# Performance work log

Measured on AMD Instinct MI355X. Metric: run time of the kernel, lower is better.

Reference implementation:

```python
import jax, jax.numpy as jnp
import numpy as np

D_MODEL = 1024
N_HEADS = 16
HEAD_DIM = D_MODEL // N_HEADS
D_FF = 4096
MAX_STEPS = 16
MAX_LEN = 64  # hardcoded in the module
LN_EPS = 1e-5


def _layer_norm(x, g, b):
    m = jnp.mean(x, axis=-1, keepdims=True)
    v = jnp.mean((x - m) ** 2, axis=-1, keepdims=True)
    return (x - m) * jax.lax.rsqrt(v + LN_EPS) * g + b


def setup_inputs() -> dict:
    key = jax.random.key(0)
    ks = jax.random.split(key, 12)
    B, S = 8, 1024
    std = 0.02
    return {
        "x": jax.random.normal(ks[0], (B, S, D_MODEL), dtype=jnp.float32),
        "step_embed": jax.random.normal(ks[1], (MAX_STEPS, D_MODEL), dtype=jnp.float32) * std,
        "qkv_w": jax.random.normal(ks[2], (D_MODEL, 3 * D_MODEL), dtype=jnp.float32) * std,
        "qkv_b": jnp.zeros((3 * D_MODEL,), dtype=jnp.float32),
        "out_w": jax.random.normal(ks[3], (D_MODEL, D_MODEL), dtype=jnp.float32) * std,
        "out_b": jnp.zeros((D_MODEL,), dtype=jnp.float32),
        "rel_pos_bias": jax.random.normal(ks[4], (2 * MAX_LEN - 1,), dtype=jnp.float32) * std,
        "w1": jax.random.normal(ks[5], (D_MODEL, D_FF), dtype=jnp.float32) * std,
        "b1": jnp.zeros((D_FF,), dtype=jnp.float32),
        "w2": jax.random.normal(ks[6], (D_FF, D_MODEL), dtype=jnp.float32) * std,
        "b2": jnp.zeros((D_MODEL,), dtype=jnp.float32),
        "ln1_g": jnp.ones((D_MODEL,), dtype=jnp.float32),
        "ln1_b": jnp.zeros((D_MODEL,), dtype=jnp.float32),
        "ln2_g": jnp.ones((D_MODEL,), dtype=jnp.float32),
        "ln2_b": jnp.zeros((D_MODEL,), dtype=jnp.float32),
        "think_step": 3,
    }


def reference(x, step_embed, qkv_w, qkv_b, out_w, out_b, rel_pos_bias,
              w1, b1, w2, b2, ln1_g, ln1_b, ln2_g, ln2_b, think_step):
    B, S, D = x.shape
    scale = HEAD_DIM ** -0.5

    # step embedding (clamped), broadcast over batch and sequence
    step = min(int(think_step), MAX_STEPS - 1)
    x = x + step_embed[step][None, None, :]

    # QKV projection -> (3, B, H, S, Dh)
    qkv = (x @ qkv_w + qkv_b).reshape(B, S, 3, N_HEADS, HEAD_DIM)
    qkv = jnp.transpose(qkv, (2, 0, 3, 1, 4))
    q, k, v = qkv[0], qkv[1], qkv[2]

    # attention scores with clamped relative-position bias
    scores = jnp.einsum("bhqd,bhkd->bhqk", q, k) * scale
    pos = jnp.arange(S)
    rel = jnp.clip(pos[:, None] - pos[None, :] + (MAX_LEN - 1), 0, 2 * MAX_LEN - 2)
    scores = scores + rel_pos_bias[rel][None, None, :, :]

    probs = jax.nn.softmax(scores, axis=-1)
    attn = jnp.einsum("bhqk,bhkd->bhqd", probs, v)
    attn = jnp.transpose(attn, (0, 2, 1, 3)).reshape(B, S, D)
    attn = attn @ out_w + out_b

    x = _layer_norm(x + attn, ln1_g, ln1_b)
    ffn = jax.nn.gelu(x @ w1 + b1, approximate=False) @ w2 + b2
    x = _layer_norm(x + ffn, ln2_g, ln2_b)
    return x
```

## Files before the change

kernel.cpp:

```cpp
#include <hip/hip_runtime.h>
#include <cstdint>
#include <cmath>

typedef unsigned short u16;
typedef unsigned int u32;
typedef __bf16 bf16x8 __attribute__((ext_vector_type(8)));
typedef float f32x4 __attribute__((ext_vector_type(4)));
typedef float f32x16 __attribute__((ext_vector_type(16)));

#define DEV __device__ __forceinline__

DEV u16 f2bf(float f) {
    union { float f; unsigned u; } a; a.f = f;
    unsigned u = a.u;
    return (u16)((u + 0x7FFFu + ((u >> 16) & 1u)) >> 16);
}

DEV u32 pack2bf(float a, float b) {
    union { float f; u32 u; } ua, ub; ua.f = a; ub.f = b;
    return __builtin_amdgcn_perm(ub.u + 0x8000u, ua.u + 0x8000u, 0x07060302u);
}

DEV float fast_exp2(float x) {
    float r;
    asm("v_exp_f32 %0, %1" : "=v"(r) : "v"(x));
    return r;
}

DEV float fast_rcp(float x) {
    float r;
    asm("v_rcp_f32 %0, %1" : "=v"(r) : "v"(x));
    return r;
}

DEV float gelu_fast(float v) {
    float z = fabsf(v) * 0.70710678118f;
    float t = fast_rcp(1.f + 0.3275911f * z);
    float poly = ((((1.061405429f * t - 1.453152027f) * t + 1.421413741f) * t
                   - 0.284496736f) * t + 0.254829592f) * t;
    float e = fast_exp2(-z * z * 1.44269504088896f);
    float erfv = 1.f - poly * e;
    erfv = copysignf(erfv, v);
    return 0.5f * v * (1.f + erfv);
}

DEV void async16(void* lds, const void* g) {
    __builtin_amdgcn_global_load_lds(
        (const __attribute__((address_space(1))) unsigned int*)g,
        (__attribute__((address_space(3))) unsigned int*)lds, 16, 0, 0);
}

#define LOG2E 1.44269504088896f
#define PHI()   __builtin_amdgcn_s_setprio(1)
#define PLO()   __builtin_amdgcn_s_setprio(0)

__global__ __launch_bounds__(256)
void prep_k(const float* __restrict__ s0, u16* __restrict__ d0,
            const float* __restrict__ s1, u16* __restrict__ d1,
            const float* __restrict__ s2, u16* __restrict__ d2,
            const float* __restrict__ s3, u16* __restrict__ d3,
            const float* __restrict__ x, const float* __restrict__ se,
            const int* __restrict__ ts, u16* __restrict__ xb) {
    int b = blockIdx.x, tid = threadIdx.x;
    if (b < 12288) {
        __shared__ float tile[32][33];
        const float* src; u16* dst; int N, tidx;
        if (b < 3072)      { src = s0; dst = d0; N = 3072; tidx = b; }
        else if (b < 4096) { src = s1; dst = d1; N = 1024; tidx = b - 3072; }
        else if (b < 8192) { src = s2; dst = d2; N = 4096; tidx = b - 4096; }
        else               { src = s3; dst = d3; N = 1024; tidx = b - 8192; }
        int ntx = N >> 5;
        int n0 = (tidx % ntx) * 32, k0 = (tidx / ntx) * 32;
        int K = (b >= 8192) ? 4096 : 1024;
        int tx = tid & 31, ty = tid >> 5;
        #pragma unroll
        for (int i = ty; i < 32; i += 8) tile[i][tx] = src[(size_t)(k0 + i) * N + n0 + tx];
        __syncthreads();
        #pragma unroll
        for (int i = ty; i < 32; i += 8) dst[(size_t)(n0 + i) * K + k0 + tx] = f2bf(tile[tx][i]);
    } else {
        int st = ts[0]; st = st < 0 ? 0 : (st > 15 ? 15 : st);
        size_t i = (size_t)(b - 12288) * 256 + tid;
        float4 v = ((const float4*)x)[i];
        int c = (int)(i & 255);
        float4 e = ((const float4*)(se + (size_t)st * 1024))[c];
        v.x += e.x; v.y += e.y; v.z += e.z; v.w += e.w;
        ushort4 u; u.x = f2bf(v.x); u.y = f2bf(v.y); u.z = f2bf(v.z); u.w = f2bf(v.w);
        ((ushort4*)xb)[i] = u;
    }
}

template<int EPI>
__global__ __launch_bounds__(256, 3)
void gemm_bt(const u16* __restrict__ A, const u16* __restrict__ Bt,
             const float* __restrict__ bias, int Kdim,
             u16* __restrict__ ob0, u16* __restrict__ ob1, u16* __restrict__ ob2,
             const float* __restrict__ addf, float* __restrict__ outf,
             const float* __restrict__ se_, const int* __restrict__ ts_) {
    __shared__ __align__(16) u16 lA[128 * 64];
    __shared__ __align__(16) u16 lB[128 * 64];
    const int tid = threadIdx.x, wave = tid >> 6, lane = tid & 63;
    const int m5 = lane & 31, h = lane >> 5;
    const int wm = wave >> 1, wn = wave & 1;
    const size_t m0 = (size_t)blockIdx.x * 128, n0 = (size_t)blockIdx.y * 128;
    const size_t kb = (size_t)Kdim * 2;

    f32x16 acc[2][2];
    #pragma unroll
    for (int i = 0; i < 2; i++)
        #pragma unroll
        for (int j = 0; j < 2; j++)
            #pragma unroll
            for (int e = 0; e < 16; e++) acc[i][j][e] = 0.f;

    const char* Ab = (const char*)A + m0 * kb;
    const char* Bb = (const char*)Bt + n0 * kb;

    auto stage = [&](const char* srcbase, u16* ldsb, int k0) {
        #pragma unroll
        for (int j = 0; j < 4; j++) {
            int loff = wave * 4096 + j * 1024 + lane * 16;
            int L = loff >> 4, r = L >> 3, c = L & 7, g = c ^ (r & 7);
            async16((char*)ldsb + loff, srcbase + (size_t)r * kb + (size_t)k0 * 2 + g * 16);
        }
    };

    stage(Ab, lA, 0); stage(Bb, lB, 0);
    const int r7 = m5 & 7;
    for (int k0 = 0; k0 < Kdim; k0 += 64) {
        __syncthreads();
        bf16x8 af[2][4], bfr[2][4];
        #pragma unroll
        for (int ti = 0; ti < 2; ti++) {
            int rowA = wm * 64 + ti * 32 + m5;
            int rowB = wn * 64 + ti * 32 + m5;
            #pragma unroll
            for (int kh = 0; kh < 4; kh++) {
                int cs = (kh * 2 + h) ^ r7;
                af[ti][kh]  = *(const bf16x8*)((const char*)lA + rowA * 128 + cs * 16);
                bfr[ti][kh] = *(const bf16x8*)((const char*)lB + rowB * 128 + cs * 16);
            }
        }
        __syncthreads();
        if (k0 + 64 < Kdim) { stage(Ab, lA, k0 + 64); stage(Bb, lB, k0 + 64); }
        #pragma unroll
        for (int kh = 0; kh < 4; kh++)
            #pragma unroll
            for (int ti = 0; ti < 2; ti++)
                #pragma unroll
                for (int tj = 0; tj < 2; tj++)
                    acc[ti][tj] = __builtin_amdgcn_mfma_f32_32x32x16_bf16(
                        af[ti][kh], bfr[tj][kh], acc[ti][tj], 0, 0, 0);
    }

    const float* serow = nullptr;
    if constexpr (EPI == 1) {
        int st = ts_[0]; st = st < 0 ? 0 : (st > 15 ? 15 : st);
        serow = se_ + (size_t)st * 1024;
    }

    #pragma unroll
    for (int ti = 0; ti < 2; ti++) {
        #pragma unroll
        for (int tj = 0; tj < 2; tj++) {
            size_t col = n0 + wn * 64 + tj * 32 + m5;
            float bv = bias[col];
            if constexpr (EPI == 0) {
                size_t t = col >> 10, c = col & 1023, hh = c >> 6, dh = c & 63;
                #pragma unroll
                for (int g = 0; g < 4; g++) {
                    size_t row0 = m0 + wm * 64 + ti * 32 + 4 * h + 8 * g;
                    size_t bq = row0 >> 10, s0 = row0 & 1023;
                    if (t == 0) {
                        #pragma unroll
                        for (int r = 0; r < 4; r++)
                            ob0[((bq * 16 + hh) * 1024 + s0 + r) * 64 + dh] =
                                f2bf((acc[ti][tj][g * 4 + r] + bv) * 0.18033688011112f);
                    } else if (t == 1) {
                        #pragma unroll
                        for (int r = 0; r < 4; r++)
                            ob1[((bq * 16 + hh) * 1024 + s0 + r) * 64 + dh] =
                                f2bf(acc[ti][tj][g * 4 + r] + bv);
                    } else {
                        ushort4 tmp;
                        tmp.x = f2bf(acc[ti][tj][g * 4 + 0] + bv);
                        tmp.y = f2bf(acc[ti][tj][g * 4 + 1] + bv);
                        tmp.z = f2bf(acc[ti][tj][g * 4 + 2] + bv);
                        tmp.w = f2bf(acc[ti][tj][g * 4 + 3] + bv);
                        *(ushort4*)(ob2 + ((bq * 16 + hh) * 64 + dh) * 1024 + s0) = tmp;
                    }
                }
            } else if constexpr (EPI == 1) {
                float sev = serow[col];
                #pragma unroll
                for (int g = 0; g < 4; g++)
                    #pragma unroll
                    for (int r = 0; r < 4; r++) {
                        size_t row = m0 + wm * 64 + ti * 32 + 4 * h + 8 * g + r;
                        float val = acc[ti][tj][g * 4 + r] + bv;
                        size_t o = row * 1024 + col;
                        outf[o] = addf[o] + sev + val;
                    }
            } else {
                #pragma unroll
                for (int g = 0; g < 4; g++) {
                    #pragma unroll
                    for (int r = 0; r < 4; r++) {
                        size_t row = m0 + wm * 64 + ti * 32 + 4 * h + 8 * g + r;
                        float val = acc[ti][tj][g * 4 + r] + bv;
                        if constexpr (EPI == 2) {
                            ob0[row * 4096 + col] = f2bf(gelu_fast(val));
                        } else {
                            size_t o = row * 1024 + col;
                            outf[o] = addf[o] + val;
                        }
                    }
                }
            }
        }
    }
}

__global__ __launch_bounds__(256, 2)
void attn_k(const u16* __restrict__ Q, const u16* __restrict__ K_, const u16* __restrict__ Vt,
            const float* __restrict__ relb, u16* __restrict__ Out) {
    __shared__ __align__(16) u16 sP[128 * 128];
    __shared__ __align__(16) u16 sK[128 * 64];
    __shared__ __align__(16) u16 sVt[64 * 128];
    __shared__ float sL[4][128];
    __shared__ float sLinv[128];
    __shared__ float sRel[128];

    const int tid = threadIdx.x, wave = tid >> 6, lane = tid & 63;
    const int m5 = lane & 31, h = lane >> 5;
    const int bh = blockIdx.x, q0 = blockIdx.y * 128;
    const size_t base = (size_t)bh * 65536;

    if (tid < 127) sRel[tid] = relb[tid] * LOG2E;

    auto stageK = [&](int kv0) {
        const char* kbp = (const char*)(K_ + base + (size_t)kv0 * 64);
        #pragma unroll
        for (int j = 0; j < 4; j++) {
            int loff = wave * 4096 + j * 1024 + lane * 16;
            int L = loff >> 4, r = L >> 3, c = L & 7, g = c ^ (r & 7);
            async16((char*)sK + loff, kbp + (size_t)r * 128 + g * 16);
        }
    };
    auto stageV = [&](int kv0) {
        const char* vbp = (const char*)(Vt + base) + (size_t)kv0 * 2;
        #pragma unroll
        for (int j = 0; j < 4; j++) {
            int loff = wave * 4096 + j * 1024 + lane * 16;
            int L = loff >> 4, r = L >> 4, c = L & 15, g = c ^ (r & 15);
            async16((char*)sVt + loff, vbp + (size_t)r * 2048 + g * 16);
        }
    };

    {
        const char* qb = (const char*)(Q + base + (size_t)q0 * 64);
        #pragma unroll
        for (int j = 0; j < 4; j++) {
            int loff = wave * 4096 + j * 1024 + lane * 16;
            int L = loff >> 4, r = L >> 3, c = L & 7, g = c ^ (r & 7);
            async16((char*)sP + loff, qb + (size_t)r * 128 + g * 16);
        }
    }
    stageK(0); stageV(0);
    __syncthreads();

    bf16x8 qf[4][4];
    #pragma unroll
    for (int qt = 0; qt < 4; qt++) {
        int row = qt * 32 + m5;
        #pragma unroll
        for (int s = 0; s < 4; s++) {
            int cs = (2 * s + h) ^ (m5 & 7);
            qf[qt][s] = *(const bf16x8*)((const char*)sP + row * 128 + cs * 16);
        }
    }
    __syncthreads();

    const int qh = wave >> 1, dhh = wave & 1;
    f32x16 Oacc[2];
    #pragma unroll
    for (int i = 0; i < 2; i++)
        #pragma unroll
        for (int e = 0; e < 16; e++) Oacc[i][e] = 0.f;
    float lsum[4] = {0.f, 0.f, 0.f, 0.f};

    for (int t = 0; t < 8; t++) {
        const int kv0 = t * 128;
        const int kvr = wave * 32 + m5;
        bf16x8 kf[4];
        #pragma unroll
        for (int s = 0; s < 4; s++) {
            int cs = (2 * s + h) ^ (m5 & 7);
            kf[s] = *(const bf16x8*)((const char*)sK + kvr * 128 + cs * 16);
        }
        f32x16 sc[4];
        #pragma unroll
        for (int qt = 0; qt < 4; qt++)
            #pragma unroll
            for (int e = 0; e < 16; e++) sc[qt][e] = 0.f;
        PHI();
        #pragma unroll
        for (int s = 0; s < 4; s++)
            #pragma unroll
            for (int qt = 0; qt < 4; qt++)
                sc[qt] = __builtin_amdgcn_mfma_f32_32x32x16_bf16(kf[s], qf[qt][s], sc[qt], 0, 0, 0);
        PLO();

        const int kvb = kv0 + wave * 32 + 4 * h;
        const bool far_lo = (kv0 >= q0 + 190);
        const bool far_hi = (kv0 <= q0 - 190);
        #pragma unroll
        for (int qt = 0; qt < 4; qt++) {
            const int qs = q0 + qt * 32 + m5;
            if (far_lo || far_hi) {
                float cb = far_lo ? sRel[0] : sRel[126];
                #pragma unroll
                for (int e = 0; e < 16; e++) sc[qt][e] = fast_exp2(sc[qt][e] + cb);
            } else {
                int relbase = qs - kvb + 63;
                #pragma unroll
                for (int g = 0; g < 4; g++)
                    #pragma unroll
                    for (int r = 0; r < 4; r++) {
                        int rel = relbase - 8 * g - r;
                        rel = rel < 0 ? 0 : (rel > 126 ? 126 : rel);
                        sc[qt][4 * g + r] = fast_exp2(sc[qt][4 * g + r] + sRel[rel]);
                    }
            }
            #pragma unroll
            for (int e = 0; e < 16; e++) lsum[qt] += sc[qt][e];
            u32 pk[4][2];
            #pragma unroll
            for (int g = 0; g < 4; g++) {
                pk[g][0] = pack2bf(sc[qt][4 * g + 0], sc[qt][4 * g + 1]);
                pk[g][1] = pack2bf(sc[qt][4 * g + 2], sc[qt][4 * g + 3]);
            }
            const int q = qt * 32 + m5;
            char* prow = (char*)sP + q * 256;
            #pragma unroll
            for (int u = 0; u < 2; u++) {
                u32 s0 = h ? pk[2 * u][0] : pk[2 * u + 1][0];
                u32 s1 = h ? pk[2 * u][1] : pk[2 * u + 1][1];
                u32 r0 = __shfl_xor((int)s0, 32);
                u32 r1 = __shfl_xor((int)s1, 32);
                uint4 w;
                if (h == 0) { w.x = pk[2 * u][0]; w.y = pk[2 * u][1]; w.z = r0; w.w = r1; }
                else        { w.x = r0; w.y = r1; w.z = pk[2 * u + 1][0]; w.w = pk[2 * u + 1][1]; }
                int c16 = (4 * wave + 2 * u + h) ^ (q & 15);
                *(uint4*)(prow + c16 * 16) = w;
            }
        }
        __syncthreads();
        if (t < 7) stageK(kv0 + 128);

        #pragma unroll
        for (int s = 0; s < 8; s++) {
            int dh = dhh * 32 + m5;
            int cv = (2 * s + h) ^ (dh & 15);
            bf16x8 vf = *(const bf16x8*)((const char*)sVt + dh * 256 + cv * 16);
            #pragma unroll
            for (int qt = 0; qt < 2; qt++) {
                int q = qh * 64 + qt * 32 + m5;
                int cp = (2 * s + h) ^ (q & 15);
                bf16x8 pf = *(const bf16x8*)((const char*)sP + q * 256 + cp * 16);
                PHI();
                Oacc[qt] = __builtin_amdgcn_mfma_f32_32x32x16_bf16(pf, vf, Oacc[qt], 0, 0, 0);
                PLO();
            }
        }
        __syncthreads();
        if (t < 7) stageV(kv0 + 128);
    }

    #pragma unroll
    for (int qt = 0; qt < 4; qt++) lsum[qt] += __shfl_xor(lsum[qt], 32);
    if (h == 0) {
        #pragma unroll
        for (int qt = 0; qt < 4; qt++) sL[wave][qt * 32 + m5] = lsum[qt];
    }
    __syncthreads();
    if (tid < 128) sLinv[tid] = 1.f / (sL[0][tid] + sL[1][tid] + sL[2][tid] + sL[3][tid]);
    __syncthreads();

    const int b = bh >> 4, hh = bh & 15;
    const int dh = dhh * 32 + m5;
    #pragma unroll
    for (int qt = 0; qt < 2; qt++) {
        #pragma unroll
        for (int g = 0; g < 4; g++) {
            #pragma unroll
            for (int r = 0; r < 4; r++) {
                int rl = qh * 64 + qt * 32 + 4 * h + 8 * g + r;
                float val = Oacc[qt][4 * g + r] * sLinv[rl];
                size_t s = (size_t)(q0 + rl);
                Out[((size_t)b * 1024 + s) * 1024 + hh * 64 + dh] = f2bf(val);
            }
        }
    }
}

template<bool WB>
__global__ __launch_bounds__(256)
void ln_k(const float* __restrict__ in, const float* __restrict__ g, const float* __restrict__ b,
          float* __restrict__ of, u16* __restrict__ ob) {
    __shared__ float ws1[4], ws2[4];
    int row = blockIdx.x, t = threadIdx.x;
    float4 v = ((const float4*)(in + (size_t)row * 1024))[t];
    float s = v.x + v.y + v.z + v.w;
    float s2 = v.x * v.x + v.y * v.y + v.z * v.z + v.w * v.w;
    #pragma unroll
    for (int m = 1; m < 64; m <<= 1) { s += __shfl_xor(s, m); s2 += __shfl_xor(s2, m); }
    if ((t & 63) == 0) { ws1[t >> 6] = s; ws2[t >> 6] = s2; }
    __syncthreads();
    s = ws1[0] + ws1[1] + ws1[2] + ws1[3];
    s2 = ws2[0] + ws2[1] + ws2[2] + ws2[3];
    float mean = s * (1.f / 1024.f);
    float var = s2 * (1.f / 1024.f) - mean * mean;
    float inv = rsqrtf(var + 1e-5f);
    float4 gv = ((const float4*)g)[t], bv = ((const float4*)b)[t];
    float4 o;
    o.x = (v.x - mean) * inv * gv.x + bv.x;
    o.y = (v.y - mean) * inv * gv.y + bv.y;
    o.z = (v.z - mean) * inv * gv.z + bv.z;
    o.w = (v.w - mean) * inv * gv.w + bv.w;
    ((float4*)(of + (size_t)row * 1024))[t] = o;
    if (WB) {
        ushort4 u; u.x = f2bf(o.x); u.y = f2bf(o.y); u.z = f2bf(o.z); u.w = f2bf(o.w);
        ((ushort4*)(ob + (size_t)row * 1024))[t] = u;
    }
}

extern "C" void kernel_launch(void* const* d_in, const int* in_sizes, int n_in,
                              void* d_out, int out_size, void* d_ws, size_t ws_size,
                              hipStream_t stream) {
    (void)in_sizes; (void)n_in; (void)out_size; (void)ws_size;
    const float* x          = (const float*)d_in[0];
    const float* step_embed = (const float*)d_in[1];
    const float* qkv_w      = (const float*)d_in[2];
    const float* qkv_b      = (const float*)d_in[3];
    const float* out_w      = (const float*)d_in[4];
    const float* out_b      = (const float*)d_in[5];
    const float* relb       = (const float*)d_in[6];
    const float* w1         = (const float*)d_in[7];
    const float* b1         = (const float*)d_in[8];
    const float* w2         = (const float*)d_in[9];
    const float* b2         = (const float*)d_in[10];
    const float* ln1g       = (const float*)d_in[11];
    const float* ln1b       = (const float*)d_in[12];
    const float* ln2g       = (const float*)d_in[13];
    const float* ln2b       = (const float*)d_in[14];
    const int*   tstep      = (const int*)d_in[15];
    float* out = (float*)d_out;

    char* p = (char*)d_ws;
    u16* wt_qkv = (u16*)p; p += (size_t)3072 * 1024 * 2;
    u16* wt_out = (u16*)p; p += (size_t)1024 * 1024 * 2;
    u16* wt_w1  = (u16*)p; p += (size_t)4096 * 1024 * 2;
    u16* wt_w2  = (u16*)p; p += (size_t)1024 * 4096 * 2;
    float* y1   = (float*)p; p += (size_t)8192 * 1024 * 4;
    u16* xseb   = (u16*)p; p += (size_t)8192 * 1024 * 2;
    u16* qbuf   = (u16*)p; p += (size_t)8192 * 1024 * 2;
    u16* kbuf   = (u16*)p; p += (size_t)8192 * 1024 * 2;
    u16* attnb  = (u16*)p; p += (size_t)8192 * 1024 * 2;
    float* res1 = (float*)p; p += (size_t)8192 * 1024 * 4;
    u16*   y1b  = xseb;
    u16*   hbuf = qbuf;
    float* res2 = res1;
    u16*   vtb  = (u16*)res1;

    prep_k<<<dim3(12288 + 8192), dim3(256), 0, stream>>>(qkv_w, wt_qkv, out_w, wt_out,
                                                         w1, wt_w1, w2, wt_w2,
                                                         x, step_embed, tstep, xseb);
    gemm_bt<0><<<dim3(64, 24), dim3(256), 0, stream>>>(xseb, wt_qkv, qkv_b, 1024,
                                                       qbuf, kbuf, vtb, (const float*)nullptr, (float*)nullptr,
                                                       (const float*)nullptr, (const int*)nullptr);
    attn_k<<<dim3(128, 8), dim3(256), 0, stream>>>(qbuf, kbuf, vtb, relb, attnb);
    gemm_bt<1><<<dim3(64, 8), dim3(256), 0, stream>>>(attnb, wt_out, out_b, 1024,
                                                      (u16*)nullptr, (u16*)nullptr, (u16*)nullptr, x, res1,
                                                      step_embed, tstep);
    ln_k<true><<<dim3(8192), dim3(256), 0, stream>>>(res1, ln1g, ln1b, y1, y1b);
    gemm_bt<2><<<dim3(64, 32), dim3(256), 0, stream>>>(y1b, wt_w1, b1, 1024,
                                                       hbuf, (u16*)nullptr, (u16*)nullptr, (const float*)nullptr, (float*)nullptr,
                                                       (const float*)nullptr, (const int*)nullptr);
    gemm_bt<3><<<dim3(64, 8), dim3(256), 0, stream>>>(hbuf, wt_w2, b2, 4096,
                                                      (u16*)nullptr, (u16*)nullptr, (u16*)nullptr, y1, res2,
                                                      (const float*)nullptr, (const int*)nullptr);
    ln_k<false><<<dim3(8192), dim3(256), 0, stream>>>(res2, ln2g, ln2b, out, (u16*)nullptr);
}
```

Baseline: 500.4 us.

## Recompute LN1 output in FFN2 epilogue from row stats; raise GEMM occupancy

The first layer norm now writes only its bf16 output plus per-row mean and inverse std. The FFN2 GEMM epilogue rebuilds the fp32 normalized residual from the res1 buffer and those stats, so the separate fp32 y1 buffer is no longer written and read back. The GEMM main loop is also restructured so LDS fragments are loaded and consumed in stages, cutting live registers, and launch bounds rise from 3 to 4 blocks per CU. The risk is register spills under the tighter bound and extra per-element loads of stats and gamma/beta in the epilogue.

```diff
diff --git a/kernel.cpp b/kernel.cpp
--- a/kernel.cpp
+++ b/kernel.cpp
@@ -91,12 +91,14 @@
 }
 
 template<int EPI>
-__global__ __launch_bounds__(256, 3)
+__global__ __launch_bounds__(256, 4)
 void gemm_bt(const u16* __restrict__ A, const u16* __restrict__ Bt,
              const float* __restrict__ bias, int Kdim,
              u16* __restrict__ ob0, u16* __restrict__ ob1, u16* __restrict__ ob2,
              const float* __restrict__ addf, float* __restrict__ outf,
-             const float* __restrict__ se_, const int* __restrict__ ts_) {
+             const float* __restrict__ se_, const int* __restrict__ ts_,
+             const float2* __restrict__ lnstats, const float* __restrict__ lng,
+             const float* __restrict__ lnb) {
     __shared__ __align__(16) u16 lA[128 * 64];
     __shared__ __align__(16) u16 lB[128 * 64];
     const int tid = threadIdx.x, wave = tid >> 6, lane = tid & 63;
@@ -127,30 +129,47 @@
 
     stage(Ab, lA, 0); stage(Bb, lB, 0);
     const int r7 = m5 & 7;
+    const int rowA0 = wm * 64 + m5, rowA1 = rowA0 + 32;
+    const int rowB0 = wn * 64 + m5, rowB1 = rowB0 + 32;
     for (int k0 = 0; k0 < Kdim; k0 += 64) {
         __syncthreads();
-        bf16x8 af[2][4], bfr[2][4];
-        #pragma unroll
-        for (int ti = 0; ti < 2; ti++) {
-            int rowA = wm * 64 + ti * 32 + m5;
-            int rowB = wn * 64 + ti * 32 + m5;
-            #pragma unroll
-            for (int kh = 0; kh < 4; kh++) {
-                int cs = (kh * 2 + h) ^ r7;
-                af[ti][kh]  = *(const bf16x8*)((const char*)lA + rowA * 128 + cs * 16);
-                bfr[ti][kh] = *(const bf16x8*)((const char*)lB + rowB * 128 + cs * 16);
-            }
+        #pragma unroll
+        for (int kh = 0; kh < 2; kh++) {
+            int cs = (kh * 2 + h) ^ r7;
+            bf16x8 a0 = *(const bf16x8*)((const char*)lA + rowA0 * 128 + cs * 16);
+            bf16x8 a1 = *(const bf16x8*)((const char*)lA + rowA1 * 128 + cs * 16);
+            bf16x8 b0 = *(const bf16x8*)((const char*)lB + rowB0 * 128 + cs * 16);
+            bf16x8 b1 = *(const bf16x8*)((const char*)lB + rowB1 * 128 + cs * 16);
+            acc[0][0] = __builtin_amdgcn_mfma_f32_32x32x16_bf16(a0, b0, acc[0][0], 0, 0, 0);
+            acc[0][1] = __builtin_amdgcn_mfma_f32_32x32x16_bf16(a0, b1, acc[0][1], 0, 0, 0);
+            acc[1][0] = __builtin_amdgcn_mfma_f32_32x32x16_bf16(a1, b0, acc[1][0], 0, 0, 0);
+            acc[1][1] = __builtin_amdgcn_mfma_f32_32x32x16_bf16(a1, b1, acc[1][1], 0, 0, 0);
+        }
+        bf16x8 a2_0, a2_1, b2_0, b2_1, a3_0, a3_1, b3_0, b3_1;
+        {
+            int cs = (4 + h) ^ r7;
+            a2_0 = *(const bf16x8*)((const char*)lA + rowA0 * 128 + cs * 16);
+            a2_1 = *(const bf16x8*)((const char*)lA + rowA1 * 128 + cs * 16);
+            b2_0 = *(const bf16x8*)((const char*)lB + rowB0 * 128 + cs * 16);
+            b2_1 = *(const bf16x8*)((const char*)lB + rowB1 * 128 + cs * 16);
+        }
+        {
+            int cs = (6 + h) ^ r7;
+            a3_0 = *(const bf16x8*)((const char*)lA + rowA0 * 128 + cs * 16);
+            a3_1 = *(const bf16x8*)((const char*)lA + rowA1 * 128 + cs * 16);
+            b3_0 = *(const bf16x8*)((const char*)lB + rowB0 * 128 + cs * 16);
+            b3_1 = *(const bf16x8*)((const char*)lB + rowB1 * 128 + cs * 16);
         }
         __syncthreads();
         if (k0 + 64 < Kdim) { stage(Ab, lA, k0 + 64); stage(Bb, lB, k0 + 64); }
-        #pragma unroll
-        for (int kh = 0; kh < 4; kh++)
-            #pragma unroll
-            for (int ti = 0; ti < 2; ti++)
-                #pragma unroll
-                for (int tj = 0; tj < 2; tj++)
-                    acc[ti][tj] = __builtin_amdgcn_mfma_f32_32x32x16_bf16(
-                        af[ti][kh], bfr[tj][kh], acc[ti][tj], 0, 0, 0);
+        acc[0][0] = __builtin_amdgcn_mfma_f32_32x32x16_bf16(a2_0, b2_0, acc[0][0], 0, 0, 0);
+        acc[0][1] = __builtin_amdgcn_mfma_f32_32x32x16_bf16(a2_0, b2_1, acc[0][1], 0, 0, 0);
+        acc[1][0] = __builtin_amdgcn_mfma_f32_32x32x16_bf16(a2_1, b2_0, acc[1][0], 0, 0, 0);
+        acc[1][1] = __builtin_amdgcn_mfma_f32_32x32x16_bf16(a2_1, b2_1, acc[1][1], 0, 0, 0);
+        acc[0][0] = __builtin_amdgcn_mfma_f32_32x32x16_bf16(a3_0, b3_0, acc[0][0], 0, 0, 0);
+        acc[0][1] = __builtin_amdgcn_mfma_f32_32x32x16_bf16(a3_0, b3_1, acc[0][1], 0, 0, 0);
+        acc[1][0] = __builtin_amdgcn_mfma_f32_32x32x16_bf16(a3_1, b3_0, acc[1][0], 0, 0, 0);
+        acc[1][1] = __builtin_amdgcn_mfma_f32_32x32x16_bf16(a3_1, b3_1, acc[1][1], 0, 0, 0);
     }
 
     const float* serow = nullptr;
@@ -201,21 +220,28 @@
                         size_t o = row * 1024 + col;
                         outf[o] = addf[o] + sev + val;
                     }
-            } else {
+            } else if constexpr (EPI == 2) {
                 #pragma unroll
-                for (int g = 0; g < 4; g++) {
+                for (int g = 0; g < 4; g++)
                     #pragma unroll
                     for (int r = 0; r < 4; r++) {
                         size_t row = m0 + wm * 64 + ti * 32 + 4 * h + 8 * g + r;
                         float val = acc[ti][tj][g * 4 + r] + bv;
-                        if constexpr (EPI == 2) {
-                            ob0[row * 4096 + col] = f2bf(gelu_fast(val));
-                        } else {
-                            size_t o = row * 1024 + col;
-                            outf[o] = addf[o] + val;
-                        }
+                        ob0[row * 4096 + col] = f2bf(gelu_fast(val));
                     }
-                }
+            } else {
+                float gv_ = lng[col], bv_ = lnb[col];
+                #pragma unroll
+                for (int g = 0; g < 4; g++)
+                    #pragma unroll
+                    for (int r = 0; r < 4; r++) {
+                        size_t row = m0 + wm * 64 + ti * 32 + 4 * h + 8 * g + r;
+                        float val = acc[ti][tj][g * 4 + r] + bv;
+                        size_t o = row * 1024 + col;
+                        float2 st = lnstats[row];
+                        float yv = (addf[o] - st.x) * st.y * gv_ + bv_;
+                        outf[o] = yv + val;
+                    }
             }
         }
     }
@@ -404,10 +430,10 @@
     }
 }
 
-template<bool WB>
+template<int MODE>
 __global__ __launch_bounds__(256)
 void ln_k(const float* __restrict__ in, const float* __restrict__ g, const float* __restrict__ b,
-          float* __restrict__ of, u16* __restrict__ ob) {
+          float* __restrict__ of, u16* __restrict__ ob, float2* __restrict__ stats) {
     __shared__ float ws1[4], ws2[4];
     int row = blockIdx.x, t = threadIdx.x;
     float4 v = ((const float4*)(in + (size_t)row * 1024))[t];
@@ -428,10 +454,12 @@
     o.y = (v.y - mean) * inv * gv.y + bv.y;
     o.z = (v.z - mean) * inv * gv.z + bv.z;
     o.w = (v.w - mean) * inv * gv.w + bv.w;
-    ((float4*)(of + (size_t)row * 1024))[t] = o;
-    if (WB) {
+    if constexpr (MODE == 0) {
+        ((float4*)(of + (size_t)row * 1024))[t] = o;
+    } else {
         ushort4 u; u.x = f2bf(o.x); u.y = f2bf(o.y); u.z = f2bf(o.z); u.w = f2bf(o.w);
         ((ushort4*)(ob + (size_t)row * 1024))[t] = u;
+        if (t == 0) stats[row] = make_float2(mean, inv);
     }
 }
 
@@ -462,11 +490,12 @@
     u16* wt_out = (u16*)p; p += (size_t)1024 * 1024 * 2;
     u16* wt_w1  = (u16*)p; p += (size_t)4096 * 1024 * 2;
     u16* wt_w2  = (u16*)p; p += (size_t)1024 * 4096 * 2;
-    float* y1   = (float*)p; p += (size_t)8192 * 1024 * 4;
+    float2* lnstats = (float2*)p; p += (size_t)8192 * 8;
     u16* xseb   = (u16*)p; p += (size_t)8192 * 1024 * 2;
     u16* qbuf   = (u16*)p; p += (size_t)8192 * 1024 * 2;
     u16* kbuf   = (u16*)p; p += (size_t)8192 * 1024 * 2;
     u16* attnb  = (u16*)p; p += (size_t)8192 * 1024 * 2;
+    p += (size_t)8192 * 1024 * 2;
     float* res1 = (float*)p; p += (size_t)8192 * 1024 * 4;
     u16*   y1b  = xseb;
     u16*   hbuf = qbuf;
@@ -478,17 +507,21 @@
                                                          x, step_embed, tstep, xseb);
     gemm_bt<0><<<dim3(64, 24), dim3(256), 0, stream>>>(xseb, wt_qkv, qkv_b, 1024,
                                                        qbuf, kbuf, vtb, (const float*)nullptr, (float*)nullptr,
-                                                       (const float*)nullptr, (const int*)nullptr);
+                                                       (const float*)nullptr, (const int*)nullptr,
+                                                       (const float2*)nullptr, (const float*)nullptr, (const float*)nullptr);
     attn_k<<<dim3(128, 8), dim3(256), 0, stream>>>(qbuf, kbuf, vtb, relb, attnb);
     gemm_bt<1><<<dim3(64, 8), dim3(256), 0, stream>>>(attnb, wt_out, out_b, 1024,
                                                       (u16*)nullptr, (u16*)nullptr, (u16*)nullptr, x, res1,
-                                                      step_embed, tstep);
-    ln_k<true><<<dim3(8192), dim3(256), 0, stream>>>(res1, ln1g, ln1b, y1, y1b);
+                                                      step_embed, tstep,
+                                                      (const float2*)nullptr, (const float*)nullptr, (const float*)nullptr);
+    ln_k<1><<<dim3(8192), dim3(256), 0, stream>>>(res1, ln1g, ln1b, (float*)nullptr, y1b, lnstats);
     gemm_bt<2><<<dim3(64, 32), dim3(256), 0, stream>>>(y1b, wt_w1, b1, 1024,
                                                        hbuf, (u16*)nullptr, (u16*)nullptr, (const float*)nullptr, (float*)nullptr,
-                                                       (const float*)nullptr, (const int*)nullptr);
+                                                       (const float*)nullptr, (const int*)nullptr,
+                                                       (const float2*)nullptr, (const float*)nullptr, (const float*)nullptr);
     gemm_bt<3><<<dim3(64, 8), dim3(256), 0, stream>>>(hbuf, wt_w2, b2, 4096,
-                                                      (u16*)nullptr, (u16*)nullptr, (u16*)nullptr, y1, res2,
-                                                      (const float*)nullptr, (const int*)nullptr);
-    ln_k<false><<<dim3(8192), dim3(256), 0, stream>>>(res2, ln2g, ln2b, out, (u16*)nullptr);
-}
+                                                      (u16*)nullptr, (u16*)nullptr, (u16*)nullptr, res1, res2,
+                                                      (const float*)nullptr, (const int*)nullptr,
+                                                      lnstats, ln1g, ln1b);
+    ln_k<0><<<dim3(8192), dim3(256), 0, stream>>>(res2, ln2g, ln2b, out, (u16*)nullptr, (float2*)nullptr);
+}
```

After: 523.1 us. 4.5% more time.
